# Performance work log

Hardware: AMD Instinct MI355X
Metric: run time of the kernel (lower is better)

Reference implementation:

```python
import jax, jax.numpy as jnp
import numpy as np

B, N = 64, 4096

def setup_inputs() -> dict:
    key = jax.random.key(0)
    k1, k2, k3, k4, k5, k6 = jax.random.split(key, 6)
    return {
        "V_mag": jax.random.uniform(k1, (B, N), dtype=jnp.float32, minval=0.9, maxval=1.1),
        "V_ang": 0.3 * jax.random.normal(k2, (B, N), dtype=jnp.float32),
        "P_in": jax.random.normal(k3, (B, N), dtype=jnp.float32),
        "Q_in": jax.random.normal(k4, (B, N), dtype=jnp.float32),
        "G_bus": jax.random.normal(k5, (N, N), dtype=jnp.float32) / np.sqrt(N),
        "B_bus": jax.random.normal(k6, (N, N), dtype=jnp.float32) / np.sqrt(N),
    }

def reference(V_mag, V_ang, P_in, Q_in, G_bus, B_bus):
    # P_i = V_i sum_j V_j (G_ij cos(ti-tj) + B_ij sin(ti-tj))
    # Q_i = V_i sum_j V_j (G_ij sin(ti-tj) - B_ij cos(ti-tj))
    # Angle-addition rewrite (exact): with c_j = V_j cos(t_j), s_j = V_j sin(t_j):
    #   sum_j G_ij V_j cos(ti-tj) = cos(ti)*(G c)_i + sin(ti)*(G s)_i, etc.
    cos_t = jnp.cos(V_ang)  # [B, N]
    sin_t = jnp.sin(V_ang)
    c = V_mag * cos_t       # V_j cos(t_j)
    s = V_mag * sin_t       # V_j sin(t_j)
    Gc = jnp.einsum('ij,bj->bi', G_bus, c)
    Gs = jnp.einsum('ij,bj->bi', G_bus, s)
    Bc = jnp.einsum('ij,bj->bi', B_bus, c)
    Bs = jnp.einsum('ij,bj->bi', B_bus, s)
    # sum_j V_j (G cos + B sin) = cos_ti*(Gc+Bs) + sin_ti*(Gs-Bc)
    P_calc = V_mag * (cos_t * (Gc + Bs) + sin_t * (Gs - Bc))
    # sum_j V_j (G sin - B cos) = sin_ti*(Gc+Bs) - cos_ti*(Gs-Bc)
    Q_calc = V_mag * (sin_t * (Gc + Bs) - cos_t * (Gs - Bc))
    res_P = P_calc - P_in
    res_Q = Q_calc - Q_in
    return (res_P, res_Q)
```

## Files before the change

### kernel.cpp

```cpp
#include <hip/hip_runtime.h>
#include <stdint.h>

#define N_DIM 4096
#define B_DIM 64

typedef __bf16 bf16x8 __attribute__((ext_vector_type(8)));
typedef float floatx4 __attribute__((ext_vector_type(4)));

union FragU { uint4 u; bf16x8 h; };

__device__ __forceinline__ unsigned short f2bf_rne(float f) {
    unsigned int u = __float_as_uint(f);
    u += 0x7fffu + ((u >> 16) & 1u);
    return (unsigned short)(u >> 16);
}

__global__ __launch_bounds__(256) void pf_prep(
        const float* __restrict__ Vmag, const float* __restrict__ Vang,
        unsigned short* __restrict__ c_pk, unsigned short* __restrict__ s_pk,
        float* __restrict__ c_f, float* __restrict__ s_f) {
    int idx = blockIdx.x * 256 + threadIdx.x;
    int b = idx >> 12;
    int j = idx & 4095;
    float sv, cv;
    sincosf(Vang[idx], &sv, &cv);
    float v = Vmag[idx];
    float c = v * cv;
    float s = v * sv;
    c_f[idx] = c;
    s_f[idx] = s;
    int p = (((j >> 3) << 6) + b) * 8 + (j & 7);
    c_pk[p] = f2bf_rne(c);
    s_pk[p] = f2bf_rne(s);
}

__global__ __launch_bounds__(512, 2) void pf_gemm(
        const float* __restrict__ G, const float* __restrict__ Bm,
        const unsigned short* __restrict__ c_pk, const unsigned short* __restrict__ s_pk,
        const float* __restrict__ c_f, const float* __restrict__ s_f,
        const float* __restrict__ P_in, const float* __restrict__ Q_in,
        float* __restrict__ out) {
    __shared__ float red[2][8][16][65];
    const int tid = threadIdx.x;
    const int wave = tid >> 6;
    const int lane = tid & 63;
    const int n = lane & 15;
    const int quad = lane >> 4;
    const int i0 = blockIdx.x << 4;
    const int kw = wave << 9;

    const float* gp = G  + (size_t)(i0 + n) * N_DIM + kw + (quad << 3);
    const float* bp = Bm + (size_t)(i0 + n) * N_DIM + kw + (quad << 3);
    const unsigned short* cp = c_pk + ((size_t)(((kw >> 3) + quad) << 6) + n) * 8;
    const unsigned short* sp = s_pk + ((size_t)(((kw >> 3) + quad) << 6) + n) * 8;

    floatx4 accX[4], accY[4];
    #pragma unroll
    for (int t = 0; t < 4; ++t) {
        accX[t] = (floatx4){0.f, 0.f, 0.f, 0.f};
        accY[t] = (floatx4){0.f, 0.f, 0.f, 0.f};
    }

    #pragma unroll 1
    for (int it = 0; it < 16; ++it) {
        float4 g0 = *(const float4*)gp;
        float4 g1 = *(const float4*)(gp + 4);
        float4 h0 = *(const float4*)bp;
        float4 h1 = *(const float4*)(bp + 4);
        uint4 cu[4], su[4];
        #pragma unroll
        for (int t = 0; t < 4; ++t) {
            cu[t] = *(const uint4*)(cp + t * 128);
            su[t] = *(const uint4*)(sp + t * 128);
        }
        gp += 32; bp += 32;
        cp += 2048; sp += 2048;

        bf16x8 ag, ah;
        ag[0] = (__bf16)g0.x; ag[1] = (__bf16)g0.y; ag[2] = (__bf16)g0.z; ag[3] = (__bf16)g0.w;
        ag[4] = (__bf16)g1.x; ag[5] = (__bf16)g1.y; ag[6] = (__bf16)g1.z; ag[7] = (__bf16)g1.w;
        ah[0] = (__bf16)h0.x; ah[1] = (__bf16)h0.y; ah[2] = (__bf16)h0.z; ah[3] = (__bf16)h0.w;
        ah[4] = (__bf16)h1.x; ah[5] = (__bf16)h1.y; ah[6] = (__bf16)h1.z; ah[7] = (__bf16)h1.w;

        #pragma unroll
        for (int t = 0; t < 4; ++t) {
            FragU cf, sf, nf;
            cf.u = cu[t];
            sf.u = su[t];
            nf.u.x = cu[t].x ^ 0x80008000u;
            nf.u.y = cu[t].y ^ 0x80008000u;
            nf.u.z = cu[t].z ^ 0x80008000u;
            nf.u.w = cu[t].w ^ 0x80008000u;
            accX[t] = __builtin_amdgcn_mfma_f32_16x16x32_bf16(ag, cf.h, accX[t], 0, 0, 0);
            accX[t] = __builtin_amdgcn_mfma_f32_16x16x32_bf16(ah, sf.h, accX[t], 0, 0, 0);
            accY[t] = __builtin_amdgcn_mfma_f32_16x16x32_bf16(ag, sf.h, accY[t], 0, 0, 0);
            accY[t] = __builtin_amdgcn_mfma_f32_16x16x32_bf16(ah, nf.h, accY[t], 0, 0, 0);
        }
    }

    #pragma unroll
    for (int t = 0; t < 4; ++t) {
        #pragma unroll
        for (int r = 0; r < 4; ++r) {
            red[0][wave][(quad << 2) + r][(t << 4) + n] = accX[t][r];
            red[1][wave][(quad << 2) + r][(t << 4) + n] = accY[t][r];
        }
    }
    __syncthreads();

    for (int e = tid; e < 1024; e += 512) {
        int bb = e >> 4;
        int m = e & 15;
        float X = 0.f, Y = 0.f;
        #pragma unroll
        for (int w = 0; w < 8; ++w) {
            X += red[0][w][m][bb];
            Y += red[1][w][m][bb];
        }
        size_t off = (size_t)bb * N_DIM + i0 + m;
        float c = c_f[off], s = s_f[off];
        out[off] = c * X + s * Y - P_in[off];
        out[(size_t)B_DIM * N_DIM + off] = s * X - c * Y - Q_in[off];
    }
}

extern "C" void kernel_launch(void* const* d_in, const int* in_sizes, int n_in,
                              void* d_out, int out_size, void* d_ws, size_t ws_size,
                              hipStream_t stream) {
    const float* Vmag = (const float*)d_in[0];
    const float* Vang = (const float*)d_in[1];
    const float* P_in = (const float*)d_in[2];
    const float* Q_in = (const float*)d_in[3];
    const float* G    = (const float*)d_in[4];
    const float* Bm   = (const float*)d_in[5];
    float* out = (float*)d_out;

    char* ws = (char*)d_ws;
    unsigned short* c_pk = (unsigned short*)(ws);
    unsigned short* s_pk = (unsigned short*)(ws + (512u << 10));
    float* c_f = (float*)(ws + (1u << 20));
    float* s_f = (float*)(ws + (2u << 20));

    hipLaunchKernelGGL(pf_prep, dim3((B_DIM * N_DIM) / 256), dim3(256), 0, stream,
                       Vmag, Vang, c_pk, s_pk, c_f, s_f);
    hipLaunchKernelGGL(pf_gemm, dim3(N_DIM / 16), dim3(512), 0, stream,
                       G, Bm, c_pk, s_pk, c_f, s_f, P_in, Q_in, out);
}
```

Before: 166.2 us.

## Double wave count per block, prefetch G/B rows, split c/s fragment loads

Each GEMM block now has 16 waves of 1024 threads, so each wave covers half as much of the K range, which raises the number of waves in flight for latency hiding. The next iteration's G and B values are software-prefetched into registers. The c and s fragment loads are split so each group of MFMAs issues right after its own loads, which lowers register pressure. The cross-wave reduction becomes a two-stage shared-memory accumulation with an extra barrier, and the LDS row padding changes.

```diff
diff --git a/kernel.cpp b/kernel.cpp
--- a/kernel.cpp
+++ b/kernel.cpp
@@ -34,20 +34,20 @@
     s_pk[p] = f2bf_rne(s);
 }
 
-__global__ __launch_bounds__(512, 2) void pf_gemm(
+__global__ __launch_bounds__(1024, 4) void pf_gemm(
         const float* __restrict__ G, const float* __restrict__ Bm,
         const unsigned short* __restrict__ c_pk, const unsigned short* __restrict__ s_pk,
         const float* __restrict__ c_f, const float* __restrict__ s_f,
         const float* __restrict__ P_in, const float* __restrict__ Q_in,
         float* __restrict__ out) {
-    __shared__ float red[2][8][16][65];
+    __shared__ float red[2][8][16][66];
     const int tid = threadIdx.x;
     const int wave = tid >> 6;
     const int lane = tid & 63;
     const int n = lane & 15;
     const int quad = lane >> 4;
     const int i0 = blockIdx.x << 4;
-    const int kw = wave << 9;
+    const int kw = wave << 8;
 
     const float* gp = G  + (size_t)(i0 + n) * N_DIM + kw + (quad << 3);
     const float* bp = Bm + (size_t)(i0 + n) * N_DIM + kw + (quad << 3);
@@ -61,20 +61,27 @@
         accY[t] = (floatx4){0.f, 0.f, 0.f, 0.f};
     }
 
+    float4 g0 = *(const float4*)gp;
+    float4 g1 = *(const float4*)(gp + 4);
+    float4 h0 = *(const float4*)bp;
+    float4 h1 = *(const float4*)(bp + 4);
+    gp += 32; bp += 32;
+
     #pragma unroll 1
-    for (int it = 0; it < 16; ++it) {
-        float4 g0 = *(const float4*)gp;
-        float4 g1 = *(const float4*)(gp + 4);
-        float4 h0 = *(const float4*)bp;
-        float4 h1 = *(const float4*)(bp + 4);
-        uint4 cu[4], su[4];
+    for (int it = 0; it < 8; ++it) {
+        float4 ng0, ng1, nh0, nh1;
+        if (it < 7) {
+            ng0 = *(const float4*)gp;
+            ng1 = *(const float4*)(gp + 4);
+            nh0 = *(const float4*)bp;
+            nh1 = *(const float4*)(bp + 4);
+            gp += 32; bp += 32;
+        }
+
+        uint4 cu[4];
         #pragma unroll
-        for (int t = 0; t < 4; ++t) {
-            cu[t] = *(const uint4*)(cp + t * 128);
-            su[t] = *(const uint4*)(sp + t * 128);
-        }
-        gp += 32; bp += 32;
-        cp += 2048; sp += 2048;
+        for (int t = 0; t < 4; ++t) cu[t] = *(const uint4*)(cp + t * 128);
+        cp += 2048;
 
         bf16x8 ag, ah;
         ag[0] = (__bf16)g0.x; ag[1] = (__bf16)g0.y; ag[2] = (__bf16)g0.z; ag[3] = (__bf16)g0.w;
@@ -84,33 +91,58 @@
 
         #pragma unroll
         for (int t = 0; t < 4; ++t) {
-            FragU cf, sf, nf;
+            FragU cf, nf;
             cf.u = cu[t];
-            sf.u = su[t];
             nf.u.x = cu[t].x ^ 0x80008000u;
             nf.u.y = cu[t].y ^ 0x80008000u;
             nf.u.z = cu[t].z ^ 0x80008000u;
             nf.u.w = cu[t].w ^ 0x80008000u;
             accX[t] = __builtin_amdgcn_mfma_f32_16x16x32_bf16(ag, cf.h, accX[t], 0, 0, 0);
+            accY[t] = __builtin_amdgcn_mfma_f32_16x16x32_bf16(ah, nf.h, accY[t], 0, 0, 0);
+        }
+
+        uint4 su[4];
+        #pragma unroll
+        for (int t = 0; t < 4; ++t) su[t] = *(const uint4*)(sp + t * 128);
+        sp += 2048;
+
+        #pragma unroll
+        for (int t = 0; t < 4; ++t) {
+            FragU sf;
+            sf.u = su[t];
             accX[t] = __builtin_amdgcn_mfma_f32_16x16x32_bf16(ah, sf.h, accX[t], 0, 0, 0);
             accY[t] = __builtin_amdgcn_mfma_f32_16x16x32_bf16(ag, sf.h, accY[t], 0, 0, 0);
-            accY[t] = __builtin_amdgcn_mfma_f32_16x16x32_bf16(ah, nf.h, accY[t], 0, 0, 0);
+        }
+
+        if (it < 7) { g0 = ng0; g1 = ng1; h0 = nh0; h1 = nh1; }
+    }
+
+    if (wave >= 8) {
+        #pragma unroll
+        for (int t = 0; t < 4; ++t) {
+            #pragma unroll
+            for (int r = 0; r < 4; ++r) {
+                red[0][wave - 8][(quad << 2) + r][(t << 4) + n] = accX[t][r];
+                red[1][wave - 8][(quad << 2) + r][(t << 4) + n] = accY[t][r];
+            }
         }
     }
-
-    #pragma unroll
-    for (int t = 0; t < 4; ++t) {
+    __syncthreads();
+    if (wave < 8) {
         #pragma unroll
-        for (int r = 0; r < 4; ++r) {
-            red[0][wave][(quad << 2) + r][(t << 4) + n] = accX[t][r];
-            red[1][wave][(quad << 2) + r][(t << 4) + n] = accY[t][r];
+        for (int t = 0; t < 4; ++t) {
+            #pragma unroll
+            for (int r = 0; r < 4; ++r) {
+                red[0][wave][(quad << 2) + r][(t << 4) + n] += accX[t][r];
+                red[1][wave][(quad << 2) + r][(t << 4) + n] += accY[t][r];
+            }
         }
     }
     __syncthreads();
 
-    for (int e = tid; e < 1024; e += 512) {
-        int bb = e >> 4;
-        int m = e & 15;
+    {
+        int bb = tid >> 4;
+        int m = tid & 15;
         float X = 0.f, Y = 0.f;
         #pragma unroll
         for (int w = 0; w < 8; ++w) {
@@ -143,6 +175,6 @@
 
     hipLaunchKernelGGL(pf_prep, dim3((B_DIM * N_DIM) / 256), dim3(256), 0, stream,
                        Vmag, Vang, c_pk, s_pk, c_f, s_f);
-    hipLaunchKernelGGL(pf_gemm, dim3(N_DIM / 16), dim3(512), 0, stream,
+    hipLaunchKernelGGL(pf_gemm, dim3(N_DIM / 16), dim3(1024), 0, stream,
                        G, Bm, c_pk, s_pk, c_f, s_f, P_in, Q_in, out);
 }
```

New measurement: 171.9 us. 3.4% more time.

## Software-pipeline GEMM loads with register double-buffering and reorder MFMAs

Applied to the files above, without the earlier changes.

Prefetches the packed c/s fragments one iteration ahead and the G/B rows two iterations ahead into registers, so global load latency overlaps the MFMA work of the current iteration. The MFMA sequence is split into a cos pass and a sin pass so the two accumulator chains interleave. The reduction buffer padding changes from 65 to 66, and the LDS store is split by wave half with no change in what gets stored. The extra live registers may push against the 2-waves-per-SIMD launch bound and raise register pressure.

```diff
diff --git a/kernel.cpp b/kernel.cpp
--- a/kernel.cpp
+++ b/kernel.cpp
@@ -3,6 +3,7 @@
 
 #define N_DIM 4096
 #define B_DIM 64
+#define OUTSZ (B_DIM * N_DIM)
 
 typedef __bf16 bf16x8 __attribute__((ext_vector_type(8)));
 typedef float floatx4 __attribute__((ext_vector_type(4)));
@@ -40,7 +41,7 @@
         const float* __restrict__ c_f, const float* __restrict__ s_f,
         const float* __restrict__ P_in, const float* __restrict__ Q_in,
         float* __restrict__ out) {
-    __shared__ float red[2][8][16][65];
+    __shared__ float red[2][8][16][66];
     const int tid = threadIdx.x;
     const int wave = tid >> 6;
     const int lane = tid & 63;
@@ -61,50 +62,85 @@
         accY[t] = (floatx4){0.f, 0.f, 0.f, 0.f};
     }
 
+    uint4 cu0[4], su0[4], cu1[4], su1[4];
+    float4 g0a, g1a, h0a, h1a;
+    float4 g0b, g1b, h0b, h1b;
+
+    #pragma unroll
+    for (int t = 0; t < 4; ++t) cu0[t] = *(const uint4*)(cp + t * 128);
+    #pragma unroll
+    for (int t = 0; t < 4; ++t) su0[t] = *(const uint4*)(sp + t * 128);
+    g0a = *(const float4*)gp;  g1a = *(const float4*)(gp + 4);
+    h0a = *(const float4*)bp;  h1a = *(const float4*)(bp + 4);
+    g0b = *(const float4*)(gp + 32);  g1b = *(const float4*)(gp + 36);
+    h0b = *(const float4*)(bp + 32);  h1b = *(const float4*)(bp + 36);
+
     #pragma unroll 1
     for (int it = 0; it < 16; ++it) {
-        float4 g0 = *(const float4*)gp;
-        float4 g1 = *(const float4*)(gp + 4);
-        float4 h0 = *(const float4*)bp;
-        float4 h1 = *(const float4*)(bp + 4);
-        uint4 cu[4], su[4];
-        #pragma unroll
-        for (int t = 0; t < 4; ++t) {
-            cu[t] = *(const uint4*)(cp + t * 128);
-            su[t] = *(const uint4*)(sp + t * 128);
+        if (it < 15) {
+            const unsigned short* cn = cp + (it + 1) * 2048;
+            const unsigned short* sn = sp + (it + 1) * 2048;
+            #pragma unroll
+            for (int t = 0; t < 4; ++t) cu1[t] = *(const uint4*)(cn + t * 128);
+            #pragma unroll
+            for (int t = 0; t < 4; ++t) su1[t] = *(const uint4*)(sn + t * 128);
         }
-        gp += 32; bp += 32;
-        cp += 2048; sp += 2048;
+        float4 g0c, g1c, h0c, h1c;
+        if (it < 14) {
+            const float* gn = gp + (it + 2) * 32;
+            const float* bn = bp + (it + 2) * 32;
+            g0c = *(const float4*)gn;  g1c = *(const float4*)(gn + 4);
+            h0c = *(const float4*)bn;  h1c = *(const float4*)(bn + 4);
+        }
 
         bf16x8 ag, ah;
-        ag[0] = (__bf16)g0.x; ag[1] = (__bf16)g0.y; ag[2] = (__bf16)g0.z; ag[3] = (__bf16)g0.w;
-        ag[4] = (__bf16)g1.x; ag[5] = (__bf16)g1.y; ag[6] = (__bf16)g1.z; ag[7] = (__bf16)g1.w;
-        ah[0] = (__bf16)h0.x; ah[1] = (__bf16)h0.y; ah[2] = (__bf16)h0.z; ah[3] = (__bf16)h0.w;
-        ah[4] = (__bf16)h1.x; ah[5] = (__bf16)h1.y; ah[6] = (__bf16)h1.z; ah[7] = (__bf16)h1.w;
+        ag[0] = (__bf16)g0a.x; ag[1] = (__bf16)g0a.y; ag[2] = (__bf16)g0a.z; ag[3] = (__bf16)g0a.w;
+        ag[4] = (__bf16)g1a.x; ag[5] = (__bf16)g1a.y; ag[6] = (__bf16)g1a.z; ag[7] = (__bf16)g1a.w;
+        ah[0] = (__bf16)h0a.x; ah[1] = (__bf16)h0a.y; ah[2] = (__bf16)h0a.z; ah[3] = (__bf16)h0a.w;
+        ah[4] = (__bf16)h1a.x; ah[5] = (__bf16)h1a.y; ah[6] = (__bf16)h1a.z; ah[7] = (__bf16)h1a.w;
 
         #pragma unroll
         for (int t = 0; t < 4; ++t) {
-            FragU cf, sf, nf;
-            cf.u = cu[t];
-            sf.u = su[t];
-            nf.u.x = cu[t].x ^ 0x80008000u;
-            nf.u.y = cu[t].y ^ 0x80008000u;
-            nf.u.z = cu[t].z ^ 0x80008000u;
-            nf.u.w = cu[t].w ^ 0x80008000u;
+            FragU cf, nf;
+            cf.u = cu0[t];
+            nf.u.x = cu0[t].x ^ 0x80008000u;
+            nf.u.y = cu0[t].y ^ 0x80008000u;
+            nf.u.z = cu0[t].z ^ 0x80008000u;
+            nf.u.w = cu0[t].w ^ 0x80008000u;
             accX[t] = __builtin_amdgcn_mfma_f32_16x16x32_bf16(ag, cf.h, accX[t], 0, 0, 0);
+            accY[t] = __builtin_amdgcn_mfma_f32_16x16x32_bf16(ah, nf.h, accY[t], 0, 0, 0);
+        }
+        #pragma unroll
+        for (int t = 0; t < 4; ++t) {
+            FragU sf;
+            sf.u = su0[t];
             accX[t] = __builtin_amdgcn_mfma_f32_16x16x32_bf16(ah, sf.h, accX[t], 0, 0, 0);
             accY[t] = __builtin_amdgcn_mfma_f32_16x16x32_bf16(ag, sf.h, accY[t], 0, 0, 0);
-            accY[t] = __builtin_amdgcn_mfma_f32_16x16x32_bf16(ah, nf.h, accY[t], 0, 0, 0);
         }
+
+        #pragma unroll
+        for (int t = 0; t < 4; ++t) { cu0[t] = cu1[t]; su0[t] = su1[t]; }
+        g0a = g0b; g1a = g1b; h0a = h0b; h1a = h1b;
+        g0b = g0c; g1b = g1c; h0b = h0c; h1b = h1c;
     }
 
     #pragma unroll
-    for (int t = 0; t < 4; ++t) {
+    for (int t = 0; t < 4; ++t)
         #pragma unroll
         for (int r = 0; r < 4; ++r) {
-            red[0][wave][(quad << 2) + r][(t << 4) + n] = accX[t][r];
-            red[1][wave][(quad << 2) + r][(t << 4) + n] = accY[t][r];
+            if (wave >= 4) {
+                red[0][wave - 4 + 4][(quad << 2) + r][(t << 4) + n] = accX[t][r];
+                red[1][wave - 4 + 4][(quad << 2) + r][(t << 4) + n] = accY[t][r];
+            }
         }
+    if (wave >= 4) {  } else {
+        #pragma unroll
+        for (int t = 0; t < 4; ++t)
+            #pragma unroll
+            for (int r = 0; r < 4; ++r) {
+                red[0][wave][(quad << 2) + r][(t << 4) + n] = accX[t][r];
+                red[1][wave][(quad << 2) + r][(t << 4) + n] = accY[t][r];
+            }
     }
     __syncthreads();
 
@@ -120,7 +156,7 @@
         size_t off = (size_t)bb * N_DIM + i0 + m;
         float c = c_f[off], s = s_f[off];
         out[off] = c * X + s * Y - P_in[off];
-        out[(size_t)B_DIM * N_DIM + off] = s * X - c * Y - Q_in[off];
+        out[(size_t)OUTSZ + off] = s * X - c * Y - Q_in[off];
     }
 }
 
```

Result: no change. 169.3 us (+1.9%).
